# Optimization experiments

Hardware: AMD Instinct MI355X
Metric: run time of the kernel (lower is better)

## Reference

```python
import jax, jax.numpy as jnp
import numpy as np

NEG = -1e9
N_HEADS = 8

def layer_norm(x, scale, bias, eps=1e-7):
    m = x.mean(-1, keepdims=True)
    v = jnp.var(x, axis=-1, keepdims=True)
    return (x - m) * jax.lax.rsqrt(v + eps) * scale + bias

def attention(x, wqkv, wo, mask):
    B, S, H = x.shape
    dh = H // N_HEADS
    q, k, v = jnp.split(x @ wqkv, 3, axis=-1)
    hsplit = lambda t: t.reshape(B, S, N_HEADS, dh).transpose(0, 2, 1, 3)
    q, k, v = hsplit(q), hsplit(k), hsplit(v)
    scores = jnp.einsum('bhqd,bhkd->bhqk', q, k) / jnp.sqrt(jnp.float32(dh))
    probs = jax.nn.softmax(scores + mask, axis=-1)
    out = jnp.einsum('bhqk,bhkd->bhqd', probs, v).transpose(0, 2, 1, 3).reshape(B, S, H)
    return out @ wo

def encoder(x, mask, wqkv, wo, ln1, w1, w2, ln2):
    for l in range(wqkv.shape[0]):  # small fixed layer count
        x = layer_norm(x + attention(x, wqkv[l], wo[l], mask), ln1[l, 0], ln1[l, 1])
        h = jax.nn.gelu(x @ w1[l]) @ w2[l]
        x = layer_norm(x + h, ln2[l, 0], ln2[l, 1])
    return x

def setup_inputs() -> dict:
    key = jax.random.key(0)
    B, C, T, H, F, L, V = 2, 16, 64, 512, 2048, 2, 32000
    ks = iter(jax.random.split(key, 64))
    nrm = lambda shape, s=0.02: jax.random.normal(next(ks), shape, jnp.float32) * s
    lnp = lambda: jnp.stack([jnp.ones(H, jnp.float32), jnp.zeros(H, jnp.float32)])
    lnL = lambda: jnp.broadcast_to(jnp.stack([jnp.ones(H, jnp.float32), jnp.zeros(H, jnp.float32)]), (L, 2, H)) + 0.0
    num_tokens = jax.random.randint(next(ks), (B, C), 2, T + 1)
    num_chunks = jax.random.randint(next(ks), (B,), C // 2, C + 1)
    raw_ids = jax.random.randint(next(ks), (B, C, T), 1, V)
    token_ids = jnp.where(jnp.arange(T)[None, None, :] < num_tokens[:, :, None], raw_ids, 0)
    def tf(pfx):
        return {pfx + '_wqkv': nrm((L, H, 3 * H)), pfx + '_wo': nrm((L, H, H)), pfx + '_ln1': lnL(),
                pfx + '_w1': nrm((L, H, F)), pfx + '_w2': nrm((L, F, H)), pfx + '_ln2': lnL()}
    d = {'token_ids': token_ids, 'num_chunks': num_chunks, 'num_tokens': num_tokens,
         'tok_emb': nrm((V, H)), 'tok_emb_ln': lnp(), 'chunk_pos': nrm((C, H)), 'chunk_emb_ln': lnp(),
         'sos': nrm((H,)), 'dec_emb': nrm((V, H)), 'dec_emb_ln': lnp(),
         'cls_dense': nrm((H, H)), 'cls_ln': lnp(), 'cls_proj': nrm((H, V)), 'cls_b': jnp.zeros((V,), jnp.float32)}
    d.update(tf('tok')); d.update(tf('chk')); d.update(tf('dec'))
    return d

def reference(token_ids, num_chunks, num_tokens, tok_emb, tok_emb_ln, tok_wqkv, tok_wo, tok_ln1, tok_w1, tok_w2, tok_ln2, chunk_pos, chunk_emb_ln, chk_wqkv, chk_wo, chk_ln1, chk_w1, chk_w2, chk_ln2, sos, dec_emb, dec_emb_ln, dec_wqkv, dec_wo, dec_ln1, dec_w1, dec_w2, dec_ln2, cls_dense, cls_ln, cls_proj, cls_b):
    B, C, T = token_ids.shape
    H = sos.shape[0]
    S2 = C + T
    # --- token encoder over stacked chunks [B*C, T] ---
    ids = token_ids.reshape(B * C, T)
    tok_valid = jnp.arange(T)[None, :] < num_tokens.reshape(B * C, 1)
    tok_amask = jnp.where(tok_valid, 0.0, NEG)[:, None, None, :]
    x = layer_norm(tok_emb[ids], tok_emb_ln[0], tok_emb_ln[1])
    token_units = encoder(x, tok_amask, tok_wqkv, tok_wo, tok_ln1, tok_w1, tok_w2, tok_ln2)
    # --- chunk encoder (patched causal): CLS unit per chunk + chunk position embs ---
    chunk_embs = token_units.reshape(B, C, T, H)[:, :, 0, :] + chunk_pos[None]
    chunk_embs = layer_norm(chunk_embs, chunk_emb_ln[0], chunk_emb_ln[1])
    chunk_valid = jnp.arange(C)[None, :] < num_chunks[:, None]  # [B,C]
    chk_amask = jnp.where(jnp.tril(jnp.ones((C, C), bool))[None] & chunk_valid[:, None, :], 0.0, NEG)[:, None]
    chunk_units = encoder(chunk_embs, chk_amask, chk_wqkv, chk_wo, chk_ln1, chk_w1, chk_w2, chk_ln2)
    chunk_units_sos = jnp.concatenate([jnp.broadcast_to(sos, (B, 1, H)), chunk_units[:, :-1]], axis=1)
    # --- ragged decoder-input assembly (vectorized scatter replacing the double python loop) ---
    dec_tok_embs = layer_norm(dec_emb[token_ids], dec_emb_ln[0], dec_emb_ln[1])  # [B,C,T,H]
    p = jnp.arange(S2); c = jnp.arange(C); n = num_tokens
    cond_prefix = (p[None, None, :] <= c[None, :, None]) & chunk_valid[:, :, None]            # [B,C,S2]
    cond_tok = (p[None, None, :] > c[None, :, None]) & (p[None, None, :] <= c[None, :, None] + n[:, :, None]) & chunk_valid[:, :, None]
    prefix = chunk_units_sos[:, jnp.minimum(p, C - 1)]                                        # [B,S2,H]
    tidx = jnp.clip(p[None, :] - c[:, None] - 1, 0, T - 1)                                    # [C,S2]
    tok_part = jnp.take_along_axis(dec_tok_embs, jnp.broadcast_to(tidx[None, :, :, None], (B, C, S2, 1)), axis=2)
    dec_in = jnp.where(cond_prefix[..., None], prefix[:, None], 0.0) + jnp.where(cond_tok[..., None], tok_part, 0.0)
    # --- causal decoder over [B*C, C+T, H] ---
    dec_amask = jnp.where(jnp.tril(jnp.ones((S2, S2), bool)), 0.0, NEG)[None, None]
    units = encoder(dec_in.reshape(B * C, S2, H), dec_amask, dec_wqkv, dec_wo, dec_ln1, dec_w1, dec_w2, dec_ln2)
    units = units.reshape(B, C, S2, H)
    # --- ragged reassembly (vectorized gather replacing the double python loop) ---
    t = jnp.arange(T - 1)
    ridx = c[:, None] + 1 + t[None, :]  # [C,T-1], always < C+T
    gathered = jnp.take_along_axis(units, jnp.broadcast_to(ridx[None, :, :, None], (B, C, T - 1, 1)), axis=2)
    rmask = (t[None, None, :] < n[:, :, None] - 1) & chunk_valid[:, :, None]
    units_re = jnp.where(rmask[..., None], gathered, 0.0)
    # --- MLM head (cls): dense + gelu + LN + vocab projection ---
    y = layer_norm(jax.nn.gelu(units_re @ cls_dense), cls_ln[0], cls_ln[1])
    logits = y @ cls_proj + cls_b  # [B,C,T-1,V]
    return logits
```

## Files before the change

kernel.cpp:

```cpp
#include <hip/hip_runtime.h>
#include <hip/hip_bf16.h>


typedef __hip_bfloat16 bf16;
typedef __attribute__((ext_vector_type(8))) short short8;
typedef __attribute__((ext_vector_type(4))) float f32x4;

__device__ inline float b2f(bf16 x) { return __bfloat162float(x); }
__device__ inline bf16 f2b(float x) { return __float2bfloat16(x); }
__device__ inline short f2bs(float x) { bf16 h = __float2bfloat16(x); return *reinterpret_cast<short*>(&h); }
__device__ inline float gelu_f(float x) {
    return 0.5f * x * (1.f + tanhf(0.7978845608028654f * (x + 0.044715f * x * x * x)));
}
__device__ __forceinline__ void gload16(const void* g, void* l) {
    __builtin_amdgcn_global_load_lds(
        (const __attribute__((address_space(1))) unsigned int*)g,
        (__attribute__((address_space(3))) unsigned int*)l, 16, 0, 0);
}

#define NMAT 26
struct TAll {
    const float* src[NMAT];
    bf16* dst[NMAT];
    int K[NMAT], N[NMAT];
    int ofs[NMAT + 1];
};

__global__ __launch_bounds__(256) void k_transpose(TAll ta) {
    __shared__ float tile[32][33];
    int bid = blockIdx.x;
    int m = 0;
    while (m + 1 < NMAT && bid >= ta.ofs[m + 1]) ++m;
    int local = bid - ta.ofs[m];
    int K = ta.K[m], N = ta.N[m];
    int tilesX = N >> 5;
    int tx = local % tilesX, ty = local / tilesX;
    int k0 = ty << 5, n0 = tx << 5;
    const float* src = ta.src[m];
    bf16* dst = ta.dst[m];
    int t = threadIdx.x;
    int c = t & 31, r = t >> 5;
#pragma unroll
    for (int p = 0; p < 4; ++p)
        tile[r + p * 8][c] = src[(long)(k0 + r + p * 8) * N + n0 + c];
    __syncthreads();
#pragma unroll
    for (int p = 0; p < 4; ++p)
        dst[(long)(n0 + r + p * 8) * K + k0 + c] = __float2bfloat16(tile[c][r + p * 8]);
}

template<int BM, int BN, int ACT, int BIAS, int OUTBF>
__global__ __launch_bounds__(256) void k_gemm_mfma(const bf16* __restrict__ A,
        const bf16* __restrict__ Bt, const float* __restrict__ bias,
        void* __restrict__ Cc, int M, int N, int K) {
    constexpr int WM = BM / 2, WN = BN / 2, FM = WM / 16, FN = WN / 16;
    constexpr int L = BM / 32 + BN / 32;
    constexpr int ASZ = BM * 64, BSZ = BN * 64;
    __shared__ __align__(16) short As[2 * ASZ];
    __shared__ __align__(16) short Bs[2 * BSZ];
    int tid = threadIdx.x;
    int w = tid >> 6, l = tid & 63;
    int wm = w >> 1, wn = w & 1;
    int l16 = l & 15, kg = l >> 4;
    int m0 = blockIdx.y * BM, n0 = blockIdx.x * BN;
    int srow = l >> 3, scol = (l & 7) * 16;
    f32x4 acc[FM][FN];
#pragma unroll
    for (int i = 0; i < FM; ++i)
#pragma unroll
        for (int j = 0; j < FN; ++j) acc[i][j] = 0.f;

    auto stage = [&](int kt, int half) {
        long kof = (long)kt * 64;
#pragma unroll
        for (int p = 0; p < BM / 32; ++p) {
            int r = p * 32 + w * 8 + srow;
            gload16((const char*)A + (((long)(m0 + r) * K + kof) << 1) + (scol ^ ((r & 7) << 4)),
                    (char*)As + half * (ASZ * 2) + (p * 32 + w * 8) * 128);
        }
#pragma unroll
        for (int p = 0; p < BN / 32; ++p) {
            int r = p * 32 + w * 8 + srow;
            gload16((const char*)Bt + (((long)(n0 + r) * K + kof) << 1) + (scol ^ ((r & 7) << 4)),
                    (char*)Bs + half * (BSZ * 2) + (p * 32 + w * 8) * 128);
        }
    };

    int NT = K >> 6;
    stage(0, 0);
    for (int t = 0; t < NT; ++t) {
        int cur = t & 1;
        if (t + 1 < NT) {
            stage(t + 1, cur ^ 1);
            if constexpr (L == 4)      asm volatile("s_waitcnt vmcnt(4)" ::: "memory");
            else if constexpr (L == 6) asm volatile("s_waitcnt vmcnt(6)" ::: "memory");
            else                       asm volatile("s_waitcnt vmcnt(8)" ::: "memory");
        } else {
            asm volatile("s_waitcnt vmcnt(0)" ::: "memory");
        }
        __builtin_amdgcn_s_barrier();
        const char* Ab = (const char*)As + cur * (ASZ * 2);
        const char* Bb = (const char*)Bs + cur * (BSZ * 2);
#pragma unroll
        for (int ks = 0; ks < 2; ++ks) {
            short8 a[FM], b[FN];
#pragma unroll
            for (int i = 0; i < FM; ++i) {
                int ar = wm * WM + i * 16 + l16;
                a[i] = *reinterpret_cast<const short8*>(Ab + ar * 128 + ((ks * 64 + kg * 16) ^ ((ar & 7) << 4)));
            }
#pragma unroll
            for (int j = 0; j < FN; ++j) {
                int br = wn * WN + j * 16 + l16;
                b[j] = *reinterpret_cast<const short8*>(Bb + br * 128 + ((ks * 64 + kg * 16) ^ ((br & 7) << 4)));
            }
#pragma unroll
            for (int i = 0; i < FM; ++i)
#pragma unroll
                for (int j = 0; j < FN; ++j)
                    acc[i][j] = __builtin_amdgcn_mfma_f32_16x16x32_bf16(a[i], b[j], acc[i][j], 0, 0, 0);
        }
        asm volatile("s_waitcnt lgkmcnt(0)" ::: "memory");
        __builtin_amdgcn_sched_barrier(0);
        __builtin_amdgcn_s_barrier();
    }
#pragma unroll
    for (int i = 0; i < FM; ++i) {
#pragma unroll
        for (int jj = 0; jj < 4; ++jj) {
            int row = m0 + wm * WM + i * 16 + kg * 4 + jj;
            if (row < M) {
#pragma unroll
                for (int j = 0; j < FN; ++j) {
                    int col = n0 + wn * WN + j * 16 + l16;
                    float v = acc[i][j][jj];
                    if (BIAS) v += bias[col];
                    if (ACT) v = gelu_f(v);
                    if (OUTBF) ((bf16*)Cc)[(long)row * N + col] = f2b(v);
                    else       ((float*)Cc)[(long)row * N + col] = v;
                }
            }
        }
    }
}

template<int S>
__global__ __launch_bounds__(256) void k_attn_mfma(const bf16* __restrict__ qkv,
        bf16* __restrict__ att, const int* __restrict__ limits, int causal) {
    constexpr int KT = S / 16;
    constexpr int SP = ((S + 31) / 32) * 32;
    constexpr int KS = SP / 32;
    constexpr int SPAD = SP - KT * 16;
    __shared__ __align__(16) short Qs[S * 72];
    __shared__ __align__(16) short Ks[S * 72];
    __shared__ __align__(16) short Vt[64 * 104];
    __shared__ __align__(16) short Pw[4][16 * 104];
    int seq = blockIdx.x >> 3, h = blockIdx.x & 7;
    int tid = threadIdx.x;
    const short* base = (const short*)qkv + (long)seq * S * 1536 + h * 64;
    for (int idx = tid; idx < S * 8; idx += 256) {
        int i = idx >> 3, c = idx & 7;
        const short* r = base + (long)i * 1536 + c * 8;
        *reinterpret_cast<short8*>(&Qs[i * 72 + c * 8]) = *reinterpret_cast<const short8*>(r);
        *reinterpret_cast<short8*>(&Ks[i * 72 + c * 8]) = *reinterpret_cast<const short8*>(r + 512);
    }
    for (int idx = tid; idx < S * 64; idx += 256) {
        int i = idx >> 6, d = idx & 63;
        Vt[d * 104 + i] = base[(long)i * 1536 + 1024 + d];
    }
    if (SPAD > 0)
        for (int idx = tid; idx < SPAD * 64; idx += 256) {
            int d = idx >> 4, kk = idx & 15;
            Vt[d * 104 + S + kk] = 0;
        }
    __syncthreads();
    int w = tid >> 6, l = tid & 63;
    int l16 = l & 15, kg = l >> 4;
    int lim = limits ? limits[seq] : S;
    for (int qt = w; qt < KT; qt += 4) {
        f32x4 sc[KT];
#pragma unroll
        for (int kt = 0; kt < KT; ++kt) sc[kt] = 0.f;
#pragma unroll
        for (int ks = 0; ks < 2; ++ks) {
            short8 qa = *reinterpret_cast<const short8*>((const char*)Qs + (qt * 16 + l16) * 144 + ks * 64 + kg * 16);
#pragma unroll
            for (int kt = 0; kt < KT; ++kt) {
                short8 kb = *reinterpret_cast<const short8*>((const char*)Ks + (kt * 16 + l16) * 144 + ks * 64 + kg * 16);
                sc[kt] = __builtin_amdgcn_mfma_f32_16x16x32_bf16(qa, kb, sc[kt], 0, 0, 0);
            }
        }
#pragma unroll
        for (int jj = 0; jj < 4; ++jj) {
            int q = qt * 16 + kg * 4 + jj;
            float vs[KT], m = -1e30f;
#pragma unroll
            for (int kt = 0; kt < KT; ++kt) {
                int key = kt * 16 + l16;
                float s = sc[kt][jj] * 0.125f;
                bool ok = (!causal || key <= q) && (key < lim);
                vs[kt] = ok ? s : -1e30f;
                m = fmaxf(m, vs[kt]);
            }
#pragma unroll
            for (int o = 1; o < 16; o <<= 1) m = fmaxf(m, __shfl_xor(m, o));
            float sum = 0.f;
#pragma unroll
            for (int kt = 0; kt < KT; ++kt) { vs[kt] = __expf(vs[kt] - m); sum += vs[kt]; }
#pragma unroll
            for (int o = 1; o < 16; o <<= 1) sum += __shfl_xor(sum, o);
            float rinv = 1.f / sum;
#pragma unroll
            for (int kt = 0; kt < KT; ++kt)
                Pw[w][(kg * 4 + jj) * 104 + kt * 16 + l16] = f2bs(vs[kt] * rinv);
        }
        if (SPAD > 0) {
#pragma unroll
            for (int jj = 0; jj < 4; ++jj)
                Pw[w][(kg * 4 + jj) * 104 + KT * 16 + l16] = 0;
        }
        f32x4 ao[4];
#pragma unroll
        for (int ct = 0; ct < 4; ++ct) ao[ct] = 0.f;
#pragma unroll
        for (int kst = 0; kst < KS; ++kst) {
            short8 pa = *reinterpret_cast<const short8*>((const char*)&Pw[w][0] + l16 * 208 + kst * 64 + kg * 16);
#pragma unroll
            for (int ct = 0; ct < 4; ++ct) {
                short8 vb = *reinterpret_cast<const short8*>((const char*)Vt + (ct * 16 + l16) * 208 + kst * 64 + kg * 16);
                ao[ct] = __builtin_amdgcn_mfma_f32_16x16x32_bf16(pa, vb, ao[ct], 0, 0, 0);
            }
        }
#pragma unroll
        for (int ct = 0; ct < 4; ++ct)
#pragma unroll
            for (int jj = 0; jj < 4; ++jj) {
                int q = qt * 16 + kg * 4 + jj;
                att[((long)seq * S + q) * 512 + h * 64 + ct * 16 + l16] = f2b(ao[ct][jj]);
            }
    }
}

__device__ inline void ln_finish(float v0, float v1, const float* __restrict__ lnw,
                                 bf16* __restrict__ outrow) {
    float s = v0 + v1, q = v0 * v0 + v1 * v1;
#pragma unroll
    for (int o = 32; o > 0; o >>= 1) { s += __shfl_xor(s, o); q += __shfl_xor(q, o); }
    __shared__ float rs[4], rq[4];
    int w = threadIdx.x >> 6;
    if ((threadIdx.x & 63) == 0) { rs[w] = s; rq[w] = q; }
    __syncthreads();
    s = rs[0] + rs[1] + rs[2] + rs[3];
    q = rq[0] + rq[1] + rq[2] + rq[3];
    float m = s * (1.f / 512.f);
    float var = q * (1.f / 512.f) - m * m;
    float inv = rsqrtf(var + 1e-7f);
    int i0 = threadIdx.x * 2, i1 = i0 + 1;
    outrow[i0] = f2b((v0 - m) * inv * lnw[i0] + lnw[512 + i0]);
    outrow[i1] = f2b((v1 - m) * inv * lnw[i1] + lnw[512 + i1]);
}

__global__ __launch_bounds__(256) void k_embed_ln2(const int* __restrict__ ids,
        const float* __restrict__ tok_emb, const float* __restrict__ tok_lnw,
        const float* __restrict__ dec_emb, const float* __restrict__ dec_lnw,
        bf16* __restrict__ x, bf16* __restrict__ dec_tok) {
    int row = blockIdx.x;
    const float* emb; const float* lnw; bf16* out;
    if (row < 2048) { emb = tok_emb; lnw = tok_lnw; out = x + (long)row * 512; }
    else { row -= 2048; emb = dec_emb; lnw = dec_lnw; out = dec_tok + (long)row * 512; }
    const float* e = emb + (long)ids[row] * 512;
    int i0 = threadIdx.x * 2;
    ln_finish(e[i0], e[i0 + 1], lnw, out);
}

__global__ __launch_bounds__(256) void k_add_ln(const bf16* __restrict__ a, const bf16* __restrict__ b,
        const float* __restrict__ lnw, bf16* __restrict__ out) {
    int row = blockIdx.x;
    long off = (long)row * 512;
    int i0 = threadIdx.x * 2;
    float v0 = b2f(a[off + i0]), v1 = b2f(a[off + i0 + 1]);
    if (b) { v0 += b2f(b[off + i0]); v1 += b2f(b[off + i0 + 1]); }
    ln_finish(v0, v1, lnw, out + off);
}

__global__ __launch_bounds__(256) void k_chunk_ln(const bf16* __restrict__ tu, const float* __restrict__ cpos,
        const float* __restrict__ lnw, bf16* __restrict__ out) {
    int bc = blockIdx.x;
    int c = bc & 15;
    long toff = (long)bc * 64 * 512;
    int i0 = threadIdx.x * 2;
    float v0 = b2f(tu[toff + i0])     + cpos[c * 512 + i0];
    float v1 = b2f(tu[toff + i0 + 1]) + cpos[c * 512 + i0 + 1];
    ln_finish(v0, v1, lnw, out + (long)bc * 512);
}

__global__ __launch_bounds__(256) void k_dec_in(const bf16* __restrict__ chunk_units,
        const float* __restrict__ sos, const bf16* __restrict__ dec_tok,
        const int* __restrict__ num_chunks, const int* __restrict__ num_tokens,
        bf16* __restrict__ out) {
    int row = blockIdx.x;
    int p = row % 80;
    int bc = row / 80;
    int c = bc & 15, b = bc >> 4;
    int t = threadIdx.x;
    bf16* o = out + (long)row * 512;
    if (c < num_chunks[b]) {
        if (p <= c) {
            if (p == 0) {
                o[2 * t]     = f2b(sos[2 * t]);
                o[2 * t + 1] = f2b(sos[2 * t + 1]);
                return;
            }
            ((uint*)o)[t] = ((const uint*)(chunk_units + ((long)(b * 16 + p - 1)) * 512))[t];
            return;
        }
        int n = num_tokens[bc];
        if (p <= c + n) {
            ((uint*)o)[t] = ((const uint*)(dec_tok + ((long)bc * 64 + (p - c - 1)) * 512))[t];
            return;
        }
    }
    ((uint*)o)[t] = 0u;
}

__global__ __launch_bounds__(256) void k_head_gather(const bf16* __restrict__ units,
        const int* __restrict__ num_chunks, const int* __restrict__ num_tokens,
        bf16* __restrict__ out) {
    int row = blockIdx.x;
    int t = row % 63;
    int bc = row / 63;
    int c = bc & 15, b = bc >> 4;
    bool valid = (c < num_chunks[b]) && (t < num_tokens[bc] - 1);
    uint* o = (uint*)(out + (long)row * 512);
    if (valid) {
        o[threadIdx.x] = ((const uint*)(units + ((long)bc * 80 + (c + 1 + t)) * 512))[threadIdx.x];
    } else {
        o[threadIdx.x] = 0u;
    }
}

template<int S>
static void run_encoder(hipStream_t st, bf16* x, int nseq, const int* limits, int causal,
                        bf16* const* wts, const float* ln1, const float* ln2,
                        bf16* qkv, bf16* att, bf16* proj, bf16* x2, bf16* h1) {
    int R = nseq * S;
    int gy = (R + 63) / 64;
    for (int l = 0; l < 2; ++l) {
        k_gemm_mfma<64, 128, 0, 0, 1><<<dim3(12, gy), 256, 0, st>>>(x, wts[l * 4 + 0], nullptr, qkv, R, 1536, 512);
        k_attn_mfma<S><<<dim3(nseq * 8), 256, 0, st>>>(qkv, att, limits, causal);
        k_gemm_mfma<64, 64, 0, 0, 1><<<dim3(8, gy), 256, 0, st>>>(att, wts[l * 4 + 1], nullptr, proj, R, 512, 512);
        k_add_ln<<<dim3(R), 256, 0, st>>>(x, proj, ln1 + (long)l * 1024, x2);
        k_gemm_mfma<64, 128, 1, 0, 1><<<dim3(16, gy), 256, 0, st>>>(x2, wts[l * 4 + 2], nullptr, h1, R, 2048, 512);
        k_gemm_mfma<64, 64, 0, 0, 1><<<dim3(8, gy), 256, 0, st>>>(h1, wts[l * 4 + 3], nullptr, proj, R, 512, 2048);
        k_add_ln<<<dim3(R), 256, 0, st>>>(x2, proj, ln2 + (long)l * 1024, x);
    }
}

extern "C" void kernel_launch(void* const* d_in, const int* in_sizes, int n_in,
                              void* d_out, int out_size, void* d_ws, size_t ws_size,
                              hipStream_t stream) {
    (void)in_sizes; (void)n_in; (void)out_size; (void)ws_size;
    const int*   token_ids    = (const int*)d_in[0];
    const int*   num_chunks   = (const int*)d_in[1];
    const int*   num_tokens   = (const int*)d_in[2];
    const float* tok_emb      = (const float*)d_in[3];
    const float* tok_emb_ln   = (const float*)d_in[4];
    const float* chunk_pos    = (const float*)d_in[5];
    const float* chunk_emb_ln = (const float*)d_in[6];
    const float* sos          = (const float*)d_in[7];
    const float* dec_emb      = (const float*)d_in[8];
    const float* dec_emb_ln   = (const float*)d_in[9];
    const float* cls_dense    = (const float*)d_in[10];
    const float* cls_ln       = (const float*)d_in[11];
    const float* cls_proj     = (const float*)d_in[12];
    const float* cls_b        = (const float*)d_in[13];
    const float* w_in[3][4] = {
        {(const float*)d_in[14], (const float*)d_in[15], (const float*)d_in[17], (const float*)d_in[18]},
        {(const float*)d_in[20], (const float*)d_in[21], (const float*)d_in[23], (const float*)d_in[24]},
        {(const float*)d_in[26], (const float*)d_in[27], (const float*)d_in[29], (const float*)d_in[30]},
    };
    const float* ln_in[3][2] = {
        {(const float*)d_in[16], (const float*)d_in[19]},
        {(const float*)d_in[22], (const float*)d_in[25]},
        {(const float*)d_in[28], (const float*)d_in[31]},
    };

    char* p = (char*)d_ws;
    auto carve_b = [&](size_t elems) {
        bf16* r = (bf16*)p;
        p += ((elems * 2 + 255) / 256) * 256;
        return r;
    };
    bf16* x       = carve_b((size_t)2560 * 512);
    bf16* qkv     = carve_b((size_t)2560 * 1536);
    bf16* att     = carve_b((size_t)2560 * 512);
    bf16* proj    = carve_b((size_t)2560 * 512);
    bf16* x2      = carve_b((size_t)2560 * 512);
    bf16* h1      = carve_b((size_t)2560 * 2048);
    bf16* chunk_x = carve_b((size_t)64 * 512);
    bf16* dec_tok = carve_b((size_t)2048 * 512);
    bf16* unitsre = carve_b((size_t)2048 * 512);
    bf16* hbuf    = carve_b((size_t)2048 * 512);
    bf16* ybuf    = carve_b((size_t)2048 * 512);

    TAll ta;
    int nm = 0, tiles = 0;
    auto push = [&](const float* src, int K, int N) -> bf16* {
        bf16* dst = carve_b((size_t)K * N);
        ta.src[nm] = src; ta.dst[nm] = dst; ta.K[nm] = K; ta.N[nm] = N;
        ta.ofs[nm] = tiles;
        tiles += (K / 32) * (N / 32);
        ++nm;
        return dst;
    };
    static const int KN[4][2] = {{512, 1536}, {512, 512}, {512, 2048}, {2048, 512}};
    bf16* wt[3][8];
    for (int tf = 0; tf < 3; ++tf)
        for (int l = 0; l < 2; ++l)
            for (int m = 0; m < 4; ++m) {
                int K = KN[m][0], N = KN[m][1];
                wt[tf][l * 4 + m] = push(w_in[tf][m] + (long)l * K * N, K, N);
            }
    bf16* wt_dense = push(cls_dense, 512, 512);
    bf16* wt_proj  = push(cls_proj, 512, 32000);
    ta.ofs[nm] = tiles;

    k_transpose<<<dim3(tiles), 256, 0, stream>>>(ta);

    k_embed_ln2<<<4096, 256, 0, stream>>>(token_ids, tok_emb, tok_emb_ln, dec_emb, dec_emb_ln, x, dec_tok);

    run_encoder<64>(stream, x, 32, num_tokens, 0, wt[0], ln_in[0][0], ln_in[0][1],
                    qkv, att, proj, x2, h1);
    k_chunk_ln<<<32, 256, 0, stream>>>(x, chunk_pos, chunk_emb_ln, chunk_x);
    run_encoder<16>(stream, chunk_x, 2, num_chunks, 1, wt[1], ln_in[1][0], ln_in[1][1],
                    qkv, att, proj, x2, h1);
    k_dec_in<<<2560, 256, 0, stream>>>(chunk_x, sos, dec_tok, num_chunks, num_tokens, x);
    run_encoder<80>(stream, x, 32, nullptr, 1, wt[2], ln_in[2][0], ln_in[2][1],
                    qkv, att, proj, x2, h1);
    k_head_gather<<<2016, 256, 0, stream>>>(x, num_chunks, num_tokens, unitsre);
    k_gemm_mfma<64, 64, 1, 0, 1><<<dim3(8, 32), 256, 0, stream>>>(unitsre, wt_dense, nullptr, hbuf, 2016, 512, 512);
    k_add_ln<<<2016, 256, 0, stream>>>(hbuf, nullptr, cls_ln, ybuf);
    k_gemm_mfma<128, 128, 0, 1, 0><<<dim3(250, 16), 256, 0, stream>>>(ybuf, wt_proj, cls_b, d_out, 2016, 32000, 512);
}
```

Baseline: 611.2 us.

## Split attention per query tile, emit transposed V from QKV GEMM, retile GEMMs

The QKV GEMM epilogue now writes V directly in a transposed per-head layout, so attention no longer stages Q, K and V through shared memory. Attention runs one 64-thread block per (sequence, head, query tile) and reads Q, K and V^T straight from global memory, which gives many more blocks. The encoder GEMMs switch to smaller tiles (64x64 and 32x64) to fill more CUs, and the vocab-projection GEMM gets a grouped tile-order swizzle for L2 reuse. In exchange, the V^T epilogue does scattered 2-byte stores, and K is reread from global memory by every query-tile block.

```diff
diff --git a/kernel.cpp b/kernel.cpp
--- a/kernel.cpp
+++ b/kernel.cpp
@@ -49,20 +49,29 @@
         dst[(long)(n0 + r + p * 8) * K + k0 + c] = __float2bfloat16(tile[c][r + p * 8]);
 }
 
-template<int BM, int BN, int ACT, int BIAS, int OUTBF>
+template<int BM, int BN, int ACT, int BIAS, int OUTBF, int VT = 0, int SWZ = 0>
 __global__ __launch_bounds__(256) void k_gemm_mfma(const bf16* __restrict__ A,
         const bf16* __restrict__ Bt, const float* __restrict__ bias,
-        void* __restrict__ Cc, int M, int N, int K) {
+        void* __restrict__ Cc, int M, int N, int K, bf16* __restrict__ vt, int S) {
     constexpr int WM = BM / 2, WN = BN / 2, FM = WM / 16, FN = WN / 16;
     constexpr int L = BM / 32 + BN / 32;
     constexpr int ASZ = BM * 64, BSZ = BN * 64;
     __shared__ __align__(16) short As[2 * ASZ];
     __shared__ __align__(16) short Bs[2 * BSZ];
+    int m0, n0;
+    if constexpr (SWZ) {
+        int pI = blockIdx.y * 16 + blockIdx.x;
+        int q = pI >> 7, r = pI & 127;
+        int mt = r >> 3, nt = q * 8 + (r & 7);
+        if (nt * BN >= N) return;
+        m0 = mt * BM; n0 = nt * BN;
+    } else {
+        m0 = blockIdx.y * BM; n0 = blockIdx.x * BN;
+    }
     int tid = threadIdx.x;
     int w = tid >> 6, l = tid & 63;
     int wm = w >> 1, wn = w & 1;
     int l16 = l & 15, kg = l >> 4;
-    int m0 = blockIdx.y * BM, n0 = blockIdx.x * BN;
     int srow = l >> 3, scol = (l & 7) * 16;
     f32x4 acc[FM][FN];
 #pragma unroll
@@ -92,7 +101,8 @@
         int cur = t & 1;
         if (t + 1 < NT) {
             stage(t + 1, cur ^ 1);
-            if constexpr (L == 4)      asm volatile("s_waitcnt vmcnt(4)" ::: "memory");
+            if constexpr (L == 3)      asm volatile("s_waitcnt vmcnt(3)" ::: "memory");
+            else if constexpr (L == 4) asm volatile("s_waitcnt vmcnt(4)" ::: "memory");
             else if constexpr (L == 6) asm volatile("s_waitcnt vmcnt(6)" ::: "memory");
             else                       asm volatile("s_waitcnt vmcnt(8)" ::: "memory");
         } else {
@@ -136,8 +146,16 @@
                     float v = acc[i][j][jj];
                     if (BIAS) v += bias[col];
                     if (ACT) v = gelu_f(v);
-                    if (OUTBF) ((bf16*)Cc)[(long)row * N + col] = f2b(v);
-                    else       ((float*)Cc)[(long)row * N + col] = v;
+                    if (VT && col >= 1024) {
+                        int hh = (col - 1024) >> 6, dd = (col - 1024) & 63;
+                        int sq = row / S, key = row - sq * S;
+                        int SPl = ((S + 31) >> 5) << 5;
+                        vt[(((long)sq * 8 + hh) * 64 + dd) * SPl + key] = f2b(v);
+                    } else if (OUTBF) {
+                        ((bf16*)Cc)[(long)row * N + col] = f2b(v);
+                    } else {
+                        ((float*)Cc)[(long)row * N + col] = v;
+                    }
                 }
             }
         }
@@ -145,100 +163,84 @@
 }
 
 template<int S>
-__global__ __launch_bounds__(256) void k_attn_mfma(const bf16* __restrict__ qkv,
-        bf16* __restrict__ att, const int* __restrict__ limits, int causal) {
+__global__ __launch_bounds__(64) void k_attn_mfma(const bf16* __restrict__ qkv,
+        const bf16* __restrict__ vt, bf16* __restrict__ att,
+        const int* __restrict__ limits, int causal) {
     constexpr int KT = S / 16;
     constexpr int SP = ((S + 31) / 32) * 32;
     constexpr int KS = SP / 32;
     constexpr int SPAD = SP - KT * 16;
-    __shared__ __align__(16) short Qs[S * 72];
-    __shared__ __align__(16) short Ks[S * 72];
-    __shared__ __align__(16) short Vt[64 * 104];
-    __shared__ __align__(16) short Pw[4][16 * 104];
-    int seq = blockIdx.x >> 3, h = blockIdx.x & 7;
-    int tid = threadIdx.x;
-    const short* base = (const short*)qkv + (long)seq * S * 1536 + h * 64;
-    for (int idx = tid; idx < S * 8; idx += 256) {
-        int i = idx >> 3, c = idx & 7;
-        const short* r = base + (long)i * 1536 + c * 8;
-        *reinterpret_cast<short8*>(&Qs[i * 72 + c * 8]) = *reinterpret_cast<const short8*>(r);
-        *reinterpret_cast<short8*>(&Ks[i * 72 + c * 8]) = *reinterpret_cast<const short8*>(r + 512);
-    }
-    for (int idx = tid; idx < S * 64; idx += 256) {
-        int i = idx >> 6, d = idx & 63;
-        Vt[d * 104 + i] = base[(long)i * 1536 + 1024 + d];
-    }
-    if (SPAD > 0)
-        for (int idx = tid; idx < SPAD * 64; idx += 256) {
-            int d = idx >> 4, kk = idx & 15;
-            Vt[d * 104 + S + kk] = 0;
-        }
-    __syncthreads();
-    int w = tid >> 6, l = tid & 63;
+    __shared__ __align__(16) short Pw[16 * 104];
+    int bid = blockIdx.x;
+    int qt = bid % KT;
+    int bh = bid / KT;
+    int h = bh & 7, seq = bh >> 3;
+    int l = threadIdx.x;
     int l16 = l & 15, kg = l >> 4;
     int lim = limits ? limits[seq] : S;
-    for (int qt = w; qt < KT; qt += 4) {
-        f32x4 sc[KT];
-#pragma unroll
-        for (int kt = 0; kt < KT; ++kt) sc[kt] = 0.f;
-#pragma unroll
-        for (int ks = 0; ks < 2; ++ks) {
-            short8 qa = *reinterpret_cast<const short8*>((const char*)Qs + (qt * 16 + l16) * 144 + ks * 64 + kg * 16);
-#pragma unroll
-            for (int kt = 0; kt < KT; ++kt) {
-                short8 kb = *reinterpret_cast<const short8*>((const char*)Ks + (kt * 16 + l16) * 144 + ks * 64 + kg * 16);
-                sc[kt] = __builtin_amdgcn_mfma_f32_16x16x32_bf16(qa, kb, sc[kt], 0, 0, 0);
-            }
-        }
+    const short* qk = (const short*)qkv + (long)seq * S * 1536 + h * 64;
+    const short* vb_base = (const short*)vt + ((long)(seq * 8 + h) * 64) * SP;
+
+    f32x4 sc[KT];
+#pragma unroll
+    for (int kt = 0; kt < KT; ++kt) sc[kt] = 0.f;
+#pragma unroll
+    for (int ks = 0; ks < 2; ++ks) {
+        short8 qa = *reinterpret_cast<const short8*>(qk + (long)(qt * 16 + l16) * 1536 + ks * 32 + kg * 8);
+#pragma unroll
+        for (int kt = 0; kt < KT; ++kt) {
+            short8 kb = *reinterpret_cast<const short8*>(qk + (long)(kt * 16 + l16) * 1536 + 512 + ks * 32 + kg * 8);
+            sc[kt] = __builtin_amdgcn_mfma_f32_16x16x32_bf16(qa, kb, sc[kt], 0, 0, 0);
+        }
+    }
+#pragma unroll
+    for (int jj = 0; jj < 4; ++jj) {
+        int q = qt * 16 + kg * 4 + jj;
+        float vs[KT], m = -1e30f;
+#pragma unroll
+        for (int kt = 0; kt < KT; ++kt) {
+            int key = kt * 16 + l16;
+            float s = sc[kt][jj] * 0.125f;
+            bool ok = (!causal || key <= q) && (key < lim);
+            vs[kt] = ok ? s : -1e30f;
+            m = fmaxf(m, vs[kt]);
+        }
+#pragma unroll
+        for (int o = 1; o < 16; o <<= 1) m = fmaxf(m, __shfl_xor(m, o));
+        float sum = 0.f;
+#pragma unroll
+        for (int kt = 0; kt < KT; ++kt) { vs[kt] = __expf(vs[kt] - m); sum += vs[kt]; }
+#pragma unroll
+        for (int o = 1; o < 16; o <<= 1) sum += __shfl_xor(sum, o);
+        float rinv = 1.f / sum;
+#pragma unroll
+        for (int kt = 0; kt < KT; ++kt)
+            Pw[(kg * 4 + jj) * 104 + kt * 16 + l16] = f2bs(vs[kt] * rinv);
+    }
+    if (SPAD > 0) {
+#pragma unroll
+        for (int jj = 0; jj < 4; ++jj)
+            Pw[(kg * 4 + jj) * 104 + KT * 16 + l16] = 0;
+    }
+    f32x4 ao[4];
+#pragma unroll
+    for (int ct = 0; ct < 4; ++ct) ao[ct] = 0.f;
+#pragma unroll
+    for (int kst = 0; kst < KS; ++kst) {
+        short8 pa = *reinterpret_cast<const short8*>((const char*)Pw + l16 * 208 + kst * 64 + kg * 16);
+#pragma unroll
+        for (int ct = 0; ct < 4; ++ct) {
+            short8 vbf = *reinterpret_cast<const short8*>(vb_base + (long)(ct * 16 + l16) * SP + kst * 32 + kg * 8);
+            ao[ct] = __builtin_amdgcn_mfma_f32_16x16x32_bf16(pa, vbf, ao[ct], 0, 0, 0);
+        }
+    }
+#pragma unroll
+    for (int ct = 0; ct < 4; ++ct)
 #pragma unroll
         for (int jj = 0; jj < 4; ++jj) {
             int q = qt * 16 + kg * 4 + jj;
-            float vs[KT], m = -1e30f;
-#pragma unroll
-            for (int kt = 0; kt < KT; ++kt) {
-                int key = kt * 16 + l16;
-                float s = sc[kt][jj] * 0.125f;
-                bool ok = (!causal || key <= q) && (key < lim);
-                vs[kt] = ok ? s : -1e30f;
-                m = fmaxf(m, vs[kt]);
-            }
-#pragma unroll
-            for (int o = 1; o < 16; o <<= 1) m = fmaxf(m, __shfl_xor(m, o));
-            float sum = 0.f;
-#pragma unroll
-            for (int kt = 0; kt < KT; ++kt) { vs[kt] = __expf(vs[kt] - m); sum += vs[kt]; }
-#pragma unroll
-            for (int o = 1; o < 16; o <<= 1) sum += __shfl_xor(sum, o);
-            float rinv = 1.f / sum;
-#pragma unroll
-            for (int kt = 0; kt < KT; ++kt)
-                Pw[w][(kg * 4 + jj) * 104 + kt * 16 + l16] = f2bs(vs[kt] * rinv);
-        }
-        if (SPAD > 0) {
-#pragma unroll
-            for (int jj = 0; jj < 4; ++jj)
-                Pw[w][(kg * 4 + jj) * 104 + KT * 16 + l16] = 0;
-        }
-        f32x4 ao[4];
-#pragma unroll
-        for (int ct = 0; ct < 4; ++ct) ao[ct] = 0.f;
-#pragma unroll
-        for (int kst = 0; kst < KS; ++kst) {
-            short8 pa = *reinterpret_cast<const short8*>((const char*)&Pw[w][0] + l16 * 208 + kst * 64 + kg * 16);
-#pragma unroll
-            for (int ct = 0; ct < 4; ++ct) {
-                short8 vb = *reinterpret_cast<const short8*>((const char*)Vt + (ct * 16 + l16) * 208 + kst * 64 + kg * 16);
-                ao[ct] = __builtin_amdgcn_mfma_f32_16x16x32_bf16(pa, vb, ao[ct], 0, 0, 0);
-            }
-        }
-#pragma unroll
-        for (int ct = 0; ct < 4; ++ct)
-#pragma unroll
-            for (int jj = 0; jj < 4; ++jj) {
-                int q = qt * 16 + kg * 4 + jj;
-                att[((long)seq * S + q) * 512 + h * 64 + ct * 16 + l16] = f2b(ao[ct][jj]);
-            }
-    }
+            att[((long)seq * S + q) * 512 + h * 64 + ct * 16 + l16] = f2b(ao[ct][jj]);
+        }
 }
 
 __device__ inline void ln_finish(float v0, float v1, const float* __restrict__ lnw,
@@ -342,16 +344,17 @@
 template<int S>
 static void run_encoder(hipStream_t st, bf16* x, int nseq, const int* limits, int causal,
                         bf16* const* wts, const float* ln1, const float* ln2,
-                        bf16* qkv, bf16* att, bf16* proj, bf16* x2, bf16* h1) {
+                        bf16* qkv, bf16* vt, bf16* att, bf16* proj, bf16* x2, bf16* h1) {
+    constexpr int KT = S / 16;
     int R = nseq * S;
-    int gy = (R + 63) / 64;
+    int gy64 = (R + 63) / 64, gy32 = (R + 31) / 32;
     for (int l = 0; l < 2; ++l) {
-        k_gemm_mfma<64, 128, 0, 0, 1><<<dim3(12, gy), 256, 0, st>>>(x, wts[l * 4 + 0], nullptr, qkv, R, 1536, 512);
-        k_attn_mfma<S><<<dim3(nseq * 8), 256, 0, st>>>(qkv, att, limits, causal);
-        k_gemm_mfma<64, 64, 0, 0, 1><<<dim3(8, gy), 256, 0, st>>>(att, wts[l * 4 + 1], nullptr, proj, R, 512, 512);
+        k_gemm_mfma<64, 64, 0, 0, 1, 1><<<dim3(24, gy64), 256, 0, st>>>(x, wts[l * 4 + 0], nullptr, qkv, R, 1536, 512, vt, S);
+        k_attn_mfma<S><<<dim3(nseq * 8 * KT), 64, 0, st>>>(qkv, vt, att, limits, causal);
+        k_gemm_mfma<32, 64, 0, 0, 1><<<dim3(8, gy32), 256, 0, st>>>(att, wts[l * 4 + 1], nullptr, proj, R, 512, 512, nullptr, 0);
         k_add_ln<<<dim3(R), 256, 0, st>>>(x, proj, ln1 + (long)l * 1024, x2);
-        k_gemm_mfma<64, 128, 1, 0, 1><<<dim3(16, gy), 256, 0, st>>>(x2, wts[l * 4 + 2], nullptr, h1, R, 2048, 512);
-        k_gemm_mfma<64, 64, 0, 0, 1><<<dim3(8, gy), 256, 0, st>>>(h1, wts[l * 4 + 3], nullptr, proj, R, 512, 2048);
+        k_gemm_mfma<64, 64, 1, 0, 1><<<dim3(32, gy64), 256, 0, st>>>(x2, wts[l * 4 + 2], nullptr, h1, R, 2048, 512, nullptr, 0);
+        k_gemm_mfma<32, 64, 0, 0, 1><<<dim3(8, gy32), 256, 0, st>>>(h1, wts[l * 4 + 3], nullptr, proj, R, 512, 2048, nullptr, 0);
         k_add_ln<<<dim3(R), 256, 0, st>>>(x2, proj, ln2 + (long)l * 1024, x);
     }
 }
@@ -393,6 +396,7 @@
     };
     bf16* x       = carve_b((size_t)2560 * 512);
     bf16* qkv     = carve_b((size_t)2560 * 1536);
+    bf16* vt      = carve_b((size_t)32 * 8 * 64 * 96);
     bf16* att     = carve_b((size_t)2560 * 512);
     bf16* proj    = carve_b((size_t)2560 * 512);
     bf16* x2      = carve_b((size_t)2560 * 512);
@@ -430,15 +434,15 @@
     k_embed_ln2<<<4096, 256, 0, stream>>>(token_ids, tok_emb, tok_emb_ln, dec_emb, dec_emb_ln, x, dec_tok);
 
     run_encoder<64>(stream, x, 32, num_tokens, 0, wt[0], ln_in[0][0], ln_in[0][1],
-                    qkv, att, proj, x2, h1);
+                    qkv, vt, att, proj, x2, h1);
     k_chunk_ln<<<32, 256, 0, stream>>>(x, chunk_pos, chunk_emb_ln, chunk_x);
     run_encoder<16>(stream, chunk_x, 2, num_chunks, 1, wt[1], ln_in[1][0], ln_in[1][1],
-                    qkv, att, proj, x2, h1);
+                    qkv, vt, att, proj, x2, h1);
     k_dec_in<<<2560, 256, 0, stream>>>(chunk_x, sos, dec_tok, num_chunks, num_tokens, x);
     run_encoder<80>(stream, x, 32, nullptr, 1, wt[2], ln_in[2][0], ln_in[2][1],
-                    qkv, att, proj, x2, h1);
+                    qkv, vt, att, proj, x2, h1);
     k_head_gather<<<2016, 256, 0, stream>>>(x, num_chunks, num_tokens, unitsre);
-    k_gemm_mfma<64, 64, 1, 0, 1><<<dim3(8, 32), 256, 0, stream>>>(unitsre, wt_dense, nullptr, hbuf, 2016, 512, 512);
+    k_gemm_mfma<32, 64, 1, 0, 1><<<dim3(8, 63), 256, 0, stream>>>(unitsre, wt_dense, nullptr, hbuf, 2016, 512, 512, nullptr, 0);
     k_add_ln<<<2016, 256, 0, stream>>>(hbuf, nullptr, cls_ln, ybuf);
-    k_gemm_mfma<128, 128, 0, 1, 0><<<dim3(250, 16), 256, 0, stream>>>(ybuf, wt_proj, cls_b, d_out, 2016, 32000, 512);
-}
+    k_gemm_mfma<128, 128, 0, 1, 0, 0, 1><<<dim3(16, 256), 256, 0, stream>>>(ybuf, wt_proj, cls_b, d_out, 2016, 32000, 512, nullptr, 0);
+}
```

Measured after the change: 598.6 us. 1.02x faster.
